# Kernel optimization log

Measured on AMD Instinct MI355X. Metric: run time of the kernel, lower is better.

## Reference

```python
import jax, jax.numpy as jnp
import numpy as np

N_EXPERTS = 256
NUM_POINTS = 512
BATCH = 256
SHARE_DIM = 200
BASE_DIM = 20
LABEL_LEN = 2


def setup_inputs() -> dict:
    key = jax.random.key(0)
    ks = jax.random.split(key, 12)
    s_pre = 1.0 / np.sqrt(NUM_POINTS)
    s_share = 1.0 / np.sqrt(NUM_POINTS)
    s_b1 = 1.0 / np.sqrt(SHARE_DIM)
    s_b2 = 1.0 / np.sqrt(BASE_DIM)
    return {
        "x": jax.random.normal(ks[0], (BATCH, NUM_POINTS), dtype=jnp.float32),
        "magnification": jax.random.uniform(ks[1], (N_EXPERTS, BATCH), dtype=jnp.float32),
        # 256 frozen per-expert Linear(num_points, num_points)
        "W_pre": jax.random.uniform(ks[2], (N_EXPERTS, NUM_POINTS, NUM_POINTS), jnp.float32, -s_pre, s_pre),
        "b_pre": jax.random.uniform(ks[3], (N_EXPERTS, NUM_POINTS), jnp.float32, -s_pre, s_pre),
        # shared: Linear(num_points, 200) + SELU
        "W_share": jax.random.uniform(ks[4], (NUM_POINTS, SHARE_DIM), jnp.float32, -s_share, s_share),
        "b_share": jax.random.uniform(ks[5], (SHARE_DIM,), jnp.float32, -s_share, s_share),
        # base: Linear(200,20)+SELU, Linear(20,2)+Softmax(dim=1)
        "W1": jax.random.uniform(ks[6], (SHARE_DIM, BASE_DIM), jnp.float32, -s_b1, s_b1),
        "b1": jax.random.uniform(ks[7], (BASE_DIM,), jnp.float32, -s_b1, s_b1),
        "W2": jax.random.uniform(ks[8], (BASE_DIM, LABEL_LEN), jnp.float32, -s_b2, s_b2),
        "b2": jax.random.uniform(ks[9], (LABEL_LEN,), jnp.float32, -s_b2, s_b2),
    }


def reference(x, magnification, W_pre, b_pre, W_share, b_share, W1, b1, W2, b2):
    # Batch all 256 expert evaluations as one grouped computation.
    # temp[e,b,p] = magnification[e,b] * x[b,p]
    temp = magnification[:, :, None] * x[None, :, :]            # [E,B,P]
    # per-expert frozen linear: grouped GEMM
    h = jnp.einsum("ebp,epq->ebq", temp, W_pre) + b_pre[:, None, :]   # [E,B,P]
    # shared Linear + SELU
    h = jax.nn.selu(jnp.einsum("ebp,ps->ebs", h, W_share) + b_share)  # [E,B,200]
    # base head (shared weights, applied per expert)
    h = jax.nn.selu(jnp.einsum("ebs,st->ebt", h, W1) + b1)            # [E,B,20]
    logits = jnp.einsum("ebt,tl->ebl", h, W2) + b2                    # [E,B,2]
    probs = jax.nn.softmax(logits, axis=-1)  # Softmax(dim=1) on each [B,2] block
    # torch.cat along dim 0 over the 256 experts
    return probs.reshape(N_EXPERTS * x.shape[0], LABEL_LEN)
```

## Files before the change

kernel.cpp:

```cpp
#include <hip/hip_runtime.h>
#include <hip/hip_bf16.h>


typedef float  f32x4  __attribute__((ext_vector_type(4)));
typedef __bf16 bf16x8 __attribute__((ext_vector_type(8)));
typedef __bf16 bf16x4 __attribute__((ext_vector_type(4)));
typedef int    i32x2  __attribute__((ext_vector_type(2)));
typedef int    i32x4  __attribute__((ext_vector_type(4)));

#define MFMA16(a, b, c) __builtin_amdgcn_mfma_f32_16x16x32_bf16((a), (b), (c), 0, 0, 0)

static constexpr int NB = 256, NP = 512, NS = 200;

static constexpr int ST_PITCH = 72;
static constexpr int ST_BUF   = 64 * ST_PITCH;
static constexpr int OFF_ST   = 0;
static constexpr int OFF_HT   = 9216;
static constexpr int HT_PITCH = 144;
static constexpr int H2_P     = 232;
static constexpr int OFF_H2   = 0;
static constexpr int OFF_PART = 118784;
static constexpr int SMEM_BYTES = 122880;

#define LGKM_BARRIER()                                        \
    do {                                                      \
        asm volatile("s_waitcnt lgkmcnt(0)" ::: "memory");    \
        __builtin_amdgcn_s_barrier();                         \
    } while (0)


__global__ void prep_xf(const float* __restrict__ x, __bf16* __restrict__ xf) {
    int t   = blockIdx.x * 256 + threadIdx.x;
    int l   = t & 63;
    int r16 = (t >> 6) & 15;
    int k32 = t >> 10;
    const float* src = x + (r16 * 16 + (l & 15)) * NP + k32 * 32 + (l >> 4) * 8;
    bf16x8 v;
#pragma unroll
    for (int e = 0; e < 8; e++) v[e] = (__bf16)src[e];
    *(bf16x8*)(xf + (size_t)t * 8) = v;
}

__global__ void prep_ws(const float* __restrict__ Ws, __bf16* __restrict__ wf) {
    int i = blockIdx.x * 256 + threadIdx.x;
    int e8  = i & 7;
    int l   = (i >> 3) & 63;
    int n16 = (i >> 9) % 14;
    int k32 = (i >> 9) / 14;
    int q = k32 * 32 + (l >> 4) * 8 + e8;
    int s = n16 * 16 + (l & 15);
    float v = (s < NS) ? Ws[q * NS + s] : 0.0f;
    wf[i] = (__bf16)v;
}


#define K_STEP(S, XC, XN, WLD, WUSE)                                          \
    {                                                                         \
        const int s1_ = (S) + 1, s2_ = (S) + 2;                               \
        if (s1_ < 128) {                                                      \
            const int k1_ = s1_ & 15;                                         \
            _Pragma("unroll")                                                 \
            for (int i_ = 0; i_ < 4; i_++)                                    \
                XN[i_] = *(const bf16x8*)(xfw + k1_ * 8192 + i_ * 512);       \
        }                                                                     \
        if (s2_ < 128) {                                                      \
            const int nt2_ = s2_ >> 4, k2_ = s2_ & 15;                        \
            _Pragma("unroll")                                                 \
            for (int i_ = 0; i_ < 4; i_++)                                    \
                WLD[i_] = WpreE[(size_t)(k2_ * 32 + p0 + i_) * NP + nt2_ * 64 + q]; \
        }                                                                     \
        {                                                                     \
            const char* stb_ = smem + OFF_ST + ((S) & 1) * ST_BUF;            \
            bf16x8 bf_[2];                                                    \
            _Pragma("unroll")                                                 \
            for (int j_ = 0; j_ < 2; j_++) {                                  \
                const int q_ = wc * 32 + j_ * 16 + l15;                       \
                union { i32x4 u; bf16x8 b; } cv_;                             \
                i32x2 lo_ = *(const i32x2*)(stb_ + q_ * ST_PITCH + lg * 16);  \
                i32x2 hi_ = *(const i32x2*)(stb_ + q_ * ST_PITCH + lg * 16 + 8); \
                cv_.u = (i32x4){lo_.x, lo_.y, hi_.x, hi_.y};                  \
                bf_[j_] = cv_.b;                                              \
            }                                                                 \
            _Pragma("unroll")                                                 \
            for (int i_ = 0; i_ < 4; i_++)                                    \
                _Pragma("unroll")                                             \
                for (int j_ = 0; j_ < 2; j_++)                                \
                    acc1[i_][j_] = MFMA16(XC[i_], bf_[j_], acc1[i_][j_]);     \
        }                                                                     \
        if (s1_ < 128) {                                                      \
            bf16x4 wv_;                                                       \
            _Pragma("unroll")                                                 \
            for (int i_ = 0; i_ < 4; i_++) wv_[i_] = (__bf16)WUSE[i_];        \
            *(bf16x4*)(smem + OFF_ST + (s1_ & 1) * ST_BUF + q * ST_PITCH + p0 * 2) = wv_; \
        }                                                                     \
        LGKM_BARRIER();                                                       \
    }

__global__ __launch_bounds__(512, 2) void fused_experts(
    const float* __restrict__ mag,
    const float* __restrict__ Wpre,
    const float* __restrict__ bpre,
    const float* __restrict__ bshare,
    const float* __restrict__ W1,
    const float* __restrict__ b1,
    const float* __restrict__ W2,
    const float* __restrict__ b2,
    const __bf16* __restrict__ xf,
    const __bf16* __restrict__ wsf,
    float* __restrict__ out)
{
    __shared__ __align__(16) char smem[SMEM_BYTES];

    const int e    = blockIdx.x;
    const int tid  = threadIdx.x;
    const int lane = tid & 63;
    const int wid  = tid >> 6;
    const int wr   = wid >> 1;
    const int wc   = wid & 1;
    const int l15  = lane & 15;
    const int lg   = lane >> 4;

    const int q  = tid & 63;
    const int p0 = (tid >> 6) * 4;

    const float* WpreE = Wpre + (size_t)e * NP * NP;
    const __bf16* xfw  = xf + (wr * 4 * 64 + lane) * 8;

    f32x4 magv[4];
#pragma unroll
    for (int i = 0; i < 4; i++)
        magv[i] = *(const f32x4*)(mag + e * NB + wr * 64 + i * 16 + lg * 4);

    f32x4 acc2[4][7];
#pragma unroll
    for (int i = 0; i < 4; i++)
#pragma unroll
        for (int j = 0; j < 7; j++) acc2[i][j] = (f32x4){0.f, 0.f, 0.f, 0.f};
    f32x4 acc1[4][2];
#pragma unroll
    for (int i = 0; i < 4; i++)
#pragma unroll
        for (int j = 0; j < 2; j++) acc1[i][j] = (f32x4){0.f, 0.f, 0.f, 0.f};

    bf16x8 XA[4], XB[4];
    float  WEV[4], WOD[4], WT[4];

#pragma unroll
    for (int i = 0; i < 4; i++)
        XA[i] = *(const bf16x8*)(xfw + i * 512);
#pragma unroll
    for (int i = 0; i < 4; i++)
        WT[i]  = WpreE[(size_t)(p0 + i) * NP + q];
#pragma unroll
    for (int i = 0; i < 4; i++)
        WOD[i] = WpreE[(size_t)(32 + p0 + i) * NP + q];
    {
        bf16x4 wv;
#pragma unroll
        for (int i = 0; i < 4; i++) wv[i] = (__bf16)WT[i];
        *(bf16x4*)(smem + OFF_ST + q * ST_PITCH + p0 * 2) = wv;
    }
    LGKM_BARRIER();

    __bf16* ht = (__bf16*)(smem + OFF_HT);

    for (int ss = 0; ss < 128; ss += 2) {
        K_STEP(ss,     XA, XB, WEV, WOD);
        K_STEP(ss + 1, XB, XA, WOD, WEV);

        if ((ss & 15) == 14) {
            const int nt = ss >> 4;

            const float bp0 = bpre[e * NP + nt * 64 + wc * 32 + l15];
            const float bp1 = bpre[e * NP + nt * 64 + wc * 32 + 16 + l15];
#pragma unroll
            for (int j = 0; j < 2; j++) {
                const float bp = j ? bp1 : bp0;
#pragma unroll
                for (int i = 0; i < 4; i++) {
#pragma unroll
                    for (int r = 0; r < 4; r++) {
                        const float h = magv[i][r] * acc1[i][j][r] + bp;
                        ht[(wr * 64 + i * 16 + lg * 4 + r) * 72 + wc * 32 + j * 16 + l15] = (__bf16)h;
                    }
                }
            }
            LGKM_BARRIER();

#pragma unroll
            for (int kk = 0; kk < 2; kk++) {
                bf16x8 wfr[7];
#pragma unroll
                for (int j2 = 0; j2 < 7; j2++)
                    wfr[j2] = *(const bf16x8*)(wsf +
                        (size_t)((((nt * 2 + kk) * 14) + wc * 7 + j2) * 64 + lane) * 8);
                bf16x8 a2[4];
#pragma unroll
                for (int i = 0; i < 4; i++)
                    a2[i] = *(const bf16x8*)(ht + (wr * 64 + i * 16 + l15) * 72 + kk * 32 + lg * 8);
#pragma unroll
                for (int i = 0; i < 4; i++)
#pragma unroll
                    for (int j2 = 0; j2 < 7; j2++)
                        acc2[i][j2] = MFMA16(a2[i], wfr[j2], acc2[i][j2]);
            }

#pragma unroll
            for (int i = 0; i < 4; i++)
#pragma unroll
                for (int j = 0; j < 2; j++) acc1[i][j] = (f32x4){0.f, 0.f, 0.f, 0.f};
        }
    }

    __syncthreads();

    __bf16* h2  = (__bf16*)(smem + OFF_H2);
    float* part = (float*)(smem + OFF_PART);
    const float SC = 1.0507009873554805f;
    const float AL = 1.6732632423543772f;

#pragma unroll
    for (int j2 = 0; j2 < 7; j2++) {
        const int s = wc * 112 + j2 * 16 + l15;
        const float bs = (s < NS) ? bshare[s] : 0.0f;
#pragma unroll
        for (int i = 0; i < 4; i++) {
            const int b0 = wr * 64 + i * 16 + lg * 4;
#pragma unroll
            for (int r = 0; r < 4; r++) {
                float z = acc2[i][j2][r] + bs;
                z = (z > 0.f) ? SC * z : SC * AL * (__expf(z) - 1.f);
                h2[(b0 + r) * H2_P + s] = (__bf16)z;
            }
        }
    }
    __syncthreads();

    {
        const int b  = tid & 255;
        const int th = tid >> 8;
        float u[10];
#pragma unroll
        for (int j = 0; j < 10; j++) u[j] = b1[th * 10 + j];
        for (int s8 = 0; s8 < NS; s8 += 8) {
            bf16x8 hv = *(const bf16x8*)(h2 + b * H2_P + s8);
#pragma unroll
            for (int so = 0; so < 8; so++) {
                const float v = (float)hv[so];
                const float* w1row = W1 + (s8 + so) * 20 + th * 10;
#pragma unroll
                for (int j = 0; j < 10; j++) u[j] = fmaf(v, w1row[j], u[j]);
            }
        }
        float pa = 0.f, pb = 0.f;
#pragma unroll
        for (int j = 0; j < 10; j++) {
            float v = u[j];
            v = (v > 0.f) ? SC * v : SC * AL * (__expf(v) - 1.f);
            const int t = th * 10 + j;
            pa = fmaf(v, W2[t * 2 + 0], pa);
            pb = fmaf(v, W2[t * 2 + 1], pb);
        }
        part[tid * 2 + 0] = pa;
        part[tid * 2 + 1] = pb;
    }
    __syncthreads();

    if (tid < 256) {
        const int b = tid;
        const float l0 = part[b * 2 + 0] + part[(b + 256) * 2 + 0] + b2[0];
        const float l1 = part[b * 2 + 1] + part[(b + 256) * 2 + 1] + b2[1];
        const float mx  = fmaxf(l0, l1);
        const float ex0 = __expf(l0 - mx), ex1 = __expf(l1 - mx);
        const float inv = 1.0f / (ex0 + ex1);
        out[((size_t)e * NB + b) * 2 + 0] = ex0 * inv;
        out[((size_t)e * NB + b) * 2 + 1] = ex1 * inv;
    }
}


extern "C" void kernel_launch(void* const* d_in, const int* in_sizes, int n_in,
                              void* d_out, int out_size, void* d_ws, size_t ws_size,
                              hipStream_t stream) {
    const float* x      = (const float*)d_in[0];
    const float* mag    = (const float*)d_in[1];
    const float* Wpre   = (const float*)d_in[2];
    const float* bpre   = (const float*)d_in[3];
    const float* Wshare = (const float*)d_in[4];
    const float* bshare = (const float*)d_in[5];
    const float* W1     = (const float*)d_in[6];
    const float* b1     = (const float*)d_in[7];
    const float* W2     = (const float*)d_in[8];
    const float* b2     = (const float*)d_in[9];
    float* out = (float*)d_out;

    __bf16* xf  = (__bf16*)d_ws;
    __bf16* wsf = (__bf16*)((char*)d_ws + 262144);

    prep_xf<<<64, 256, 0, stream>>>(x, xf);
    prep_ws<<<448, 256, 0, stream>>>(Wshare, wsf);
    fused_experts<<<256, 512, 0, stream>>>(mag, Wpre, bpre, bshare, W1, b1,
                                           W2, b2, xf, wsf, out);
}
```

Before: 483.4 us.

## Split each expert across two workgroups by batch half and deepen K-steps

```diff
diff --git a/kernel.cpp b/kernel.cpp
--- a/kernel.cpp
+++ b/kernel.cpp
@@ -12,15 +12,14 @@
 
 static constexpr int NB = 256, NP = 512, NS = 200;
 
-static constexpr int ST_PITCH = 72;
-static constexpr int ST_BUF   = 64 * ST_PITCH;
-static constexpr int OFF_ST   = 0;
-static constexpr int OFF_HT   = 9216;
-static constexpr int HT_PITCH = 144;
-static constexpr int H2_P     = 232;
-static constexpr int OFF_H2   = 0;
-static constexpr int OFF_PART = 118784;
-static constexpr int SMEM_BYTES = 122880;
+static constexpr int SLICE   = 4608;
+static constexpr int ST_STEP = 2 * SLICE;
+static constexpr int OFF_ST  = 0;
+static constexpr int OFF_HT  = 18432;
+static constexpr int H2_P    = 232;
+static constexpr int OFF_H2  = 0;
+static constexpr int OFF_PART = 59392;
+static constexpr int SMEM_BYTES = 61440;
 
 #define LGKM_BARRIER()                                        \
     do {                                                      \
@@ -54,30 +53,59 @@
 }
 
 
-#define K_STEP(S, XC, XN, WLD, WUSE)                                          \
+#define X_LOAD(SN, XDST)                                                      \
+    if ((SN) < 64) {                                                          \
+        const int kb_ = ((SN) & 7) * 2;                                       \
+        _Pragma("unroll")                                                     \
+        for (int kk_ = 0; kk_ < 2; kk_++)                                     \
+            _Pragma("unroll")                                                 \
+            for (int i_ = 0; i_ < 4; i_++)                                    \
+                XDST[kk_ * 4 + i_] =                                          \
+                    *(const bf16x8*)(xfw + (kb_ + kk_) * 8192 + i_ * 512);    \
+    }
+
+#define W_GATHER(S2, WDST)                                                    \
+    if ((S2) < 64) {                                                          \
+        const int nt2_ = (S2) >> 3;                                           \
+        const int kb2_ = ((S2) & 7) * 2;                                      \
+        _Pragma("unroll")                                                     \
+        for (int sub_ = 0; sub_ < 2; sub_++)                                  \
+            _Pragma("unroll")                                                 \
+            for (int pp_ = 0; pp_ < 2; pp_++)                                 \
+                _Pragma("unroll")                                             \
+                for (int i_ = 0; i_ < 4; i_++)                                \
+                    WDST[sub_ * 8 + pp_ * 4 + i_] =                           \
+                        WpreE[(size_t)((kb2_ + sub_) * 32 + pp_ * 16 + p0 + i_) * NP \
+                              + nt2_ * 64 + q];                               \
+    }
+
+#define W_WRITE(S1, WSRC)                                                     \
+    if ((S1) < 64) {                                                          \
+        char* wb_ = smem + OFF_ST + ((S1) & 1) * ST_STEP;                     \
+        _Pragma("unroll")                                                     \
+        for (int sub_ = 0; sub_ < 2; sub_++)                                  \
+            _Pragma("unroll")                                                 \
+            for (int pp_ = 0; pp_ < 2; pp_++) {                               \
+                bf16x4 wv_;                                                   \
+                _Pragma("unroll")                                             \
+                for (int i_ = 0; i_ < 4; i_++)                                \
+                    wv_[i_] = (__bf16)WSRC[sub_ * 8 + pp_ * 4 + i_];          \
+                *(bf16x4*)(wb_ + sub_ * SLICE + q * 72 + (pp_ * 16 + p0) * 2) = wv_; \
+            }                                                                 \
+    }
+
+#define STEP_MFMA(S, XC)                                                      \
     {                                                                         \
-        const int s1_ = (S) + 1, s2_ = (S) + 2;                               \
-        if (s1_ < 128) {                                                      \
-            const int k1_ = s1_ & 15;                                         \
-            _Pragma("unroll")                                                 \
-            for (int i_ = 0; i_ < 4; i_++)                                    \
-                XN[i_] = *(const bf16x8*)(xfw + k1_ * 8192 + i_ * 512);       \
-        }                                                                     \
-        if (s2_ < 128) {                                                      \
-            const int nt2_ = s2_ >> 4, k2_ = s2_ & 15;                        \
-            _Pragma("unroll")                                                 \
-            for (int i_ = 0; i_ < 4; i_++)                                    \
-                WLD[i_] = WpreE[(size_t)(k2_ * 32 + p0 + i_) * NP + nt2_ * 64 + q]; \
-        }                                                                     \
-        {                                                                     \
-            const char* stb_ = smem + OFF_ST + ((S) & 1) * ST_BUF;            \
+        const char* stb_ = smem + OFF_ST + ((S) & 1) * ST_STEP;               \
+        _Pragma("unroll")                                                     \
+        for (int kk_ = 0; kk_ < 2; kk_++) {                                   \
             bf16x8 bf_[2];                                                    \
             _Pragma("unroll")                                                 \
             for (int j_ = 0; j_ < 2; j_++) {                                  \
                 const int q_ = wc * 32 + j_ * 16 + l15;                       \
                 union { i32x4 u; bf16x8 b; } cv_;                             \
-                i32x2 lo_ = *(const i32x2*)(stb_ + q_ * ST_PITCH + lg * 16);  \
-                i32x2 hi_ = *(const i32x2*)(stb_ + q_ * ST_PITCH + lg * 16 + 8); \
+                i32x2 lo_ = *(const i32x2*)(stb_ + kk_ * SLICE + q_ * 72 + lg * 16);     \
+                i32x2 hi_ = *(const i32x2*)(stb_ + kk_ * SLICE + q_ * 72 + lg * 16 + 8); \
                 cv_.u = (i32x4){lo_.x, lo_.y, hi_.x, hi_.y};                  \
                 bf_[j_] = cv_.b;                                              \
             }                                                                 \
@@ -85,18 +113,19 @@
             for (int i_ = 0; i_ < 4; i_++)                                    \
                 _Pragma("unroll")                                             \
                 for (int j_ = 0; j_ < 2; j_++)                                \
-                    acc1[i_][j_] = MFMA16(XC[i_], bf_[j_], acc1[i_][j_]);     \
+                    acc1[i_][j_] = MFMA16(XC[kk_ * 4 + i_], bf_[j_], acc1[i_][j_]); \
         }                                                                     \
-        if (s1_ < 128) {                                                      \
-            bf16x4 wv_;                                                       \
-            _Pragma("unroll")                                                 \
-            for (int i_ = 0; i_ < 4; i_++) wv_[i_] = (__bf16)WUSE[i_];        \
-            *(bf16x4*)(smem + OFF_ST + (s1_ & 1) * ST_BUF + q * ST_PITCH + p0 * 2) = wv_; \
-        }                                                                     \
-        LGKM_BARRIER();                                                       \
-    }
-
-__global__ __launch_bounds__(512, 2) void fused_experts(
+    }
+
+#define K_STEP(S, XC, XN, WC, WN)  \
+    X_LOAD((S) + 1, XN)            \
+    W_GATHER((S) + 2, WN)          \
+    STEP_MFMA(S, XC)               \
+    W_WRITE((S) + 1, WC)           \
+    LGKM_BARRIER();
+
+
+__global__ __launch_bounds__(256, 2) void fused_experts(
     const float* __restrict__ mag,
     const float* __restrict__ Wpre,
     const float* __restrict__ bpre,
@@ -111,7 +140,9 @@
 {
     __shared__ __align__(16) char smem[SMEM_BYTES];
 
-    const int e    = blockIdx.x;
+    const int bid  = blockIdx.x;
+    const int e    = bid & 255;
+    const int mh   = bid >> 8;
     const int tid  = threadIdx.x;
     const int lane = tid & 63;
     const int wid  = tid >> 6;
@@ -120,16 +151,17 @@
     const int l15  = lane & 15;
     const int lg   = lane >> 4;
 
-    const int q  = tid & 63;
-    const int p0 = (tid >> 6) * 4;
+    const int q  = lane;
+    const int p0 = wid * 4;
 
     const float* WpreE = Wpre + (size_t)e * NP * NP;
-    const __bf16* xfw  = xf + (wr * 4 * 64 + lane) * 8;
+    const __bf16* xfw  = xf + ((mh * 8 + wr * 4) * 64 + lane) * 8;
+    __bf16* ht = (__bf16*)(smem + OFF_HT);
 
     f32x4 magv[4];
 #pragma unroll
     for (int i = 0; i < 4; i++)
-        magv[i] = *(const f32x4*)(mag + e * NB + wr * 64 + i * 16 + lg * 4);
+        magv[i] = *(const f32x4*)(mag + e * NB + mh * 128 + wr * 64 + i * 16 + lg * 4);
 
     f32x4 acc2[4][7];
 #pragma unroll
@@ -142,74 +174,67 @@
 #pragma unroll
         for (int j = 0; j < 2; j++) acc1[i][j] = (f32x4){0.f, 0.f, 0.f, 0.f};
 
-    bf16x8 XA[4], XB[4];
-    float  WEV[4], WOD[4], WT[4];
-
-#pragma unroll
-    for (int i = 0; i < 4; i++)
-        XA[i] = *(const bf16x8*)(xfw + i * 512);
-#pragma unroll
-    for (int i = 0; i < 4; i++)
-        WT[i]  = WpreE[(size_t)(p0 + i) * NP + q];
-#pragma unroll
-    for (int i = 0; i < 4; i++)
-        WOD[i] = WpreE[(size_t)(32 + p0 + i) * NP + q];
-    {
-        bf16x4 wv;
-#pragma unroll
-        for (int i = 0; i < 4; i++) wv[i] = (__bf16)WT[i];
-        *(bf16x4*)(smem + OFF_ST + q * ST_PITCH + p0 * 2) = wv;
-    }
+    bf16x8 XA[8], XB[8];
+    float  WA[16], WB[16];
+    bf16x8 wfr[14];
+
+    X_LOAD(0, XA)
+    W_GATHER(0, WA)
+    W_GATHER(1, WB)
+    W_WRITE(0, WA)
     LGKM_BARRIER();
 
-    __bf16* ht = (__bf16*)(smem + OFF_HT);
-
-    for (int ss = 0; ss < 128; ss += 2) {
-        K_STEP(ss,     XA, XB, WEV, WOD);
-        K_STEP(ss + 1, XB, XA, WOD, WEV);
-
-        if ((ss & 15) == 14) {
-            const int nt = ss >> 4;
-
-            const float bp0 = bpre[e * NP + nt * 64 + wc * 32 + l15];
-            const float bp1 = bpre[e * NP + nt * 64 + wc * 32 + 16 + l15];
-#pragma unroll
-            for (int j = 0; j < 2; j++) {
-                const float bp = j ? bp1 : bp0;
-#pragma unroll
-                for (int i = 0; i < 4; i++) {
-#pragma unroll
-                    for (int r = 0; r < 4; r++) {
-                        const float h = magv[i][r] * acc1[i][j][r] + bp;
-                        ht[(wr * 64 + i * 16 + lg * 4 + r) * 72 + wc * 32 + j * 16 + l15] = (__bf16)h;
-                    }
+    for (int nt = 0; nt < 8; ++nt) {
+        const int S0 = nt * 8;
+
+#pragma unroll
+        for (int kk = 0; kk < 2; kk++)
+#pragma unroll
+            for (int j2 = 0; j2 < 7; j2++)
+                wfr[kk * 7 + j2] = *(const bf16x8*)(wsf +
+                    (size_t)((((nt * 2 + kk) * 14) + wc * 7 + j2) * 64 + lane) * 8);
+        const float bp0 = bpre[e * NP + nt * 64 + wc * 32 + l15];
+        const float bp1 = bpre[e * NP + nt * 64 + wc * 32 + 16 + l15];
+
+        K_STEP(S0 + 0, XA, XB, WB, WA)
+        K_STEP(S0 + 1, XB, XA, WA, WB)
+        K_STEP(S0 + 2, XA, XB, WB, WA)
+        K_STEP(S0 + 3, XB, XA, WA, WB)
+        K_STEP(S0 + 4, XA, XB, WB, WA)
+        K_STEP(S0 + 5, XB, XA, WA, WB)
+        K_STEP(S0 + 6, XA, XB, WB, WA)
+        K_STEP(S0 + 7, XB, XA, WA, WB)
+
+#pragma unroll
+        for (int j = 0; j < 2; j++) {
+            const float bp = j ? bp1 : bp0;
+#pragma unroll
+            for (int i = 0; i < 4; i++)
+#pragma unroll
+                for (int r = 0; r < 4; r++) {
+                    const float h = magv[i][r] * acc1[i][j][r] + bp;
+                    ht[(wr * 64 + i * 16 + lg * 4 + r) * 72 + wc * 32 + j * 16 + l15] = (__bf16)h;
                 }
-            }
-            LGKM_BARRIER();
-
-#pragma unroll
-            for (int kk = 0; kk < 2; kk++) {
-                bf16x8 wfr[7];
+        }
+        LGKM_BARRIER();
+
+#pragma unroll
+        for (int kk = 0; kk < 2; kk++) {
+            bf16x8 a2[4];
+#pragma unroll
+            for (int i = 0; i < 4; i++)
+                a2[i] = *(const bf16x8*)(ht + (wr * 64 + i * 16 + l15) * 72 + kk * 32 + lg * 8);
+#pragma unroll
+            for (int i = 0; i < 4; i++)
 #pragma unroll
                 for (int j2 = 0; j2 < 7; j2++)
-                    wfr[j2] = *(const bf16x8*)(wsf +
-                        (size_t)((((nt * 2 + kk) * 14) + wc * 7 + j2) * 64 + lane) * 8);
-                bf16x8 a2[4];
-#pragma unroll
-                for (int i = 0; i < 4; i++)
-                    a2[i] = *(const bf16x8*)(ht + (wr * 64 + i * 16 + l15) * 72 + kk * 32 + lg * 8);
-#pragma unroll
-                for (int i = 0; i < 4; i++)
-#pragma unroll
-                    for (int j2 = 0; j2 < 7; j2++)
-                        acc2[i][j2] = MFMA16(a2[i], wfr[j2], acc2[i][j2]);
-            }
-
-#pragma unroll
-            for (int i = 0; i < 4; i++)
-#pragma unroll
-                for (int j = 0; j < 2; j++) acc1[i][j] = (f32x4){0.f, 0.f, 0.f, 0.f};
-        }
+                    acc2[i][j2] = MFMA16(a2[i], wfr[kk * 7 + j2], acc2[i][j2]);
+        }
+
+#pragma unroll
+        for (int i = 0; i < 4; i++)
+#pragma unroll
+            for (int j = 0; j < 2; j++) acc1[i][j] = (f32x4){0.f, 0.f, 0.f, 0.f};
     }
 
     __syncthreads();
@@ -237,8 +262,8 @@
     __syncthreads();
 
     {
-        const int b  = tid & 255;
-        const int th = tid >> 8;
+        const int b  = tid & 127;
+        const int th = tid >> 7;
         float u[10];
 #pragma unroll
         for (int j = 0; j < 10; j++) u[j] = b1[th * 10 + j];
@@ -266,15 +291,16 @@
     }
     __syncthreads();
 
-    if (tid < 256) {
+    if (tid < 128) {
         const int b = tid;
-        const float l0 = part[b * 2 + 0] + part[(b + 256) * 2 + 0] + b2[0];
-        const float l1 = part[b * 2 + 1] + part[(b + 256) * 2 + 1] + b2[1];
+        const float l0 = part[b * 2 + 0] + part[(b + 128) * 2 + 0] + b2[0];
+        const float l1 = part[b * 2 + 1] + part[(b + 128) * 2 + 1] + b2[1];
         const float mx  = fmaxf(l0, l1);
         const float ex0 = __expf(l0 - mx), ex1 = __expf(l1 - mx);
         const float inv = 1.0f / (ex0 + ex1);
-        out[((size_t)e * NB + b) * 2 + 0] = ex0 * inv;
-        out[((size_t)e * NB + b) * 2 + 1] = ex1 * inv;
+        const size_t g = (size_t)e * NB + mh * 128 + b;
+        out[g * 2 + 0] = ex0 * inv;
+        out[g * 2 + 1] = ex1 * inv;
     }
 }
 
@@ -299,6 +325,6 @@
 
     prep_xf<<<64, 256, 0, stream>>>(x, xf);
     prep_ws<<<448, 256, 0, stream>>>(Wshare, wsf);
-    fused_experts<<<256, 512, 0, stream>>>(mag, Wpre, bpre, bshare, W1, b1,
+    fused_experts<<<512, 256, 0, stream>>>(mag, Wpre, bpre, bshare, W1, b1,
                                            W2, b2, xf, wsf, out);
 }
```

Measured after the change: 1.351 ms. +179.4%, slower.

## Pre-convert W_pre to bf16 MFMA layout and stream via async global-to-LDS ring

Applied to the files above, without the earlier changes.

```diff
diff --git a/kernel.cpp b/kernel.cpp
--- a/kernel.cpp
+++ b/kernel.cpp
@@ -4,24 +4,19 @@
 
 typedef float  f32x4  __attribute__((ext_vector_type(4)));
 typedef __bf16 bf16x8 __attribute__((ext_vector_type(8)));
-typedef __bf16 bf16x4 __attribute__((ext_vector_type(4)));
-typedef int    i32x2  __attribute__((ext_vector_type(2)));
-typedef int    i32x4  __attribute__((ext_vector_type(4)));
 
 #define MFMA16(a, b, c) __builtin_amdgcn_mfma_f32_16x16x32_bf16((a), (b), (c), 0, 0, 0)
 
 static constexpr int NB = 256, NP = 512, NS = 200;
 
-static constexpr int ST_PITCH = 72;
-static constexpr int ST_BUF   = 64 * ST_PITCH;
-static constexpr int OFF_ST   = 0;
-static constexpr int OFF_HT   = 9216;
-static constexpr int HT_PITCH = 144;
+static constexpr int OFF_RING = 0;
+static constexpr int OFF_HT   = 49152;
 static constexpr int H2_P     = 232;
 static constexpr int OFF_H2   = 0;
 static constexpr int OFF_PART = 118784;
 static constexpr int SMEM_BYTES = 122880;
 
+#define VM_WAIT(N) asm volatile("s_waitcnt vmcnt(" #N ")" ::: "memory")
 #define LGKM_BARRIER()                                        \
     do {                                                      \
         asm volatile("s_waitcnt lgkmcnt(0)" ::: "memory");    \
@@ -53,52 +48,149 @@
     wf[i] = (__bf16)v;
 }
 
-
-#define K_STEP(S, XC, XN, WLD, WUSE)                                          \
-    {                                                                         \
-        const int s1_ = (S) + 1, s2_ = (S) + 2;                               \
-        if (s1_ < 128) {                                                      \
-            const int k1_ = s1_ & 15;                                         \
+__global__ __launch_bounds__(256) void prep_w(const float* __restrict__ Wp,
+                                              __bf16* __restrict__ wpb) {
+    __shared__ float tile[128][65];
+    const int blk = blockIdx.x;
+    const int e   = blk >> 5;
+    const int sb  = blk & 31;
+    const int nt  = sb >> 2;
+    const int kq  = sb & 3;
+    const int t   = threadIdx.x;
+    const int pr  = t >> 4;
+    const int pc  = (t & 15) * 4;
+    const float* src = Wp + (size_t)e * 262144 + (size_t)(kq * 128) * 512 + nt * 64;
+#pragma unroll
+    for (int rr = 0; rr < 8; ++rr) {
+        const int p = rr * 16 + pr;
+        f32x4 v = *(const f32x4*)(src + (size_t)p * 512 + pc);
+        tile[p][pc + 0] = v.x; tile[p][pc + 1] = v.y;
+        tile[p][pc + 2] = v.z; tile[p][pc + 3] = v.w;
+    }
+    __syncthreads();
+#pragma unroll
+    for (int ff = 0; ff < 4; ++ff) {
+        const int f   = ff * 256 + t;
+        const int l   = f & 63;
+        const int n16 = (f >> 6) & 3;
+        const int sl  = f >> 8;
+        const int lp  = sl * 32 + (l >> 4) * 8;
+        const int lq  = n16 * 16 + (l & 15);
+        bf16x8 o;
+#pragma unroll
+        for (int ee = 0; ee < 8; ++ee) o[ee] = (__bf16)tile[lp + ee][lq];
+        const size_t s = (size_t)(nt * 16 + kq * 4 + sl);
+        *(bf16x8*)(wpb + ((size_t)e * 128 + s) * 2048 + (size_t)(n16 * 64 + l) * 8) = o;
+    }
+}
+
+
+#define GLL_ISSUE(SG)                                                         \
+    __builtin_amdgcn_global_load_lds(                                         \
+        (const __attribute__((address_space(1))) unsigned int*)(wp + (size_t)(SG) * 8192), \
+        (__attribute__((address_space(3))) unsigned int*)(void*)(smem + OFF_RING + ((SG) % 6) * 8192 + wid * 1024), \
+        16, 0, 0);
+
+#define X_LOAD(SN, XD)                                                        \
+    {                                                                         \
+        const int kb_ = ((SN) & 7) * 2;                                       \
+        _Pragma("unroll")                                                     \
+        for (int kk_ = 0; kk_ < 2; kk_++)                                     \
             _Pragma("unroll")                                                 \
             for (int i_ = 0; i_ < 4; i_++)                                    \
-                XN[i_] = *(const bf16x8*)(xfw + k1_ * 8192 + i_ * 512);       \
-        }                                                                     \
-        if (s2_ < 128) {                                                      \
-            const int nt2_ = s2_ >> 4, k2_ = s2_ & 15;                        \
-            _Pragma("unroll")                                                 \
-            for (int i_ = 0; i_ < 4; i_++)                                    \
-                WLD[i_] = WpreE[(size_t)(k2_ * 32 + p0 + i_) * NP + nt2_ * 64 + q]; \
-        }                                                                     \
-        {                                                                     \
-            const char* stb_ = smem + OFF_ST + ((S) & 1) * ST_BUF;            \
+                XD[kk_ * 4 + i_] =                                            \
+                    *(const bf16x8*)(xfw + (kb_ + kk_) * 8192 + i_ * 512);    \
+    }
+
+#define STEP_MFMA(S, XC)                                                      \
+    {                                                                         \
+        const char* slab_ = smem + OFF_RING + ((S) % 6) * 8192;               \
+        _Pragma("unroll")                                                     \
+        for (int kk_ = 0; kk_ < 2; kk_++) {                                   \
             bf16x8 bf_[2];                                                    \
             _Pragma("unroll")                                                 \
-            for (int j_ = 0; j_ < 2; j_++) {                                  \
-                const int q_ = wc * 32 + j_ * 16 + l15;                       \
-                union { i32x4 u; bf16x8 b; } cv_;                             \
-                i32x2 lo_ = *(const i32x2*)(stb_ + q_ * ST_PITCH + lg * 16);  \
-                i32x2 hi_ = *(const i32x2*)(stb_ + q_ * ST_PITCH + lg * 16 + 8); \
-                cv_.u = (i32x4){lo_.x, lo_.y, hi_.x, hi_.y};                  \
-                bf_[j_] = cv_.b;                                              \
-            }                                                                 \
+            for (int j_ = 0; j_ < 2; j_++)                                    \
+                bf_[j_] = *(const bf16x8*)(slab_ + kk_ * 4096 +               \
+                               (wc * 2 + j_) * 1024 + lane * 16);             \
             _Pragma("unroll")                                                 \
             for (int i_ = 0; i_ < 4; i_++)                                    \
                 _Pragma("unroll")                                             \
                 for (int j_ = 0; j_ < 2; j_++)                                \
-                    acc1[i_][j_] = MFMA16(XC[i_], bf_[j_], acc1[i_][j_]);     \
+                    acc1[i_][j_] = MFMA16(XC[kk_ * 4 + i_], bf_[j_], acc1[i_][j_]); \
         }                                                                     \
-        if (s1_ < 128) {                                                      \
-            bf16x4 wv_;                                                       \
-            _Pragma("unroll")                                                 \
-            for (int i_ = 0; i_ < 4; i_++) wv_[i_] = (__bf16)WUSE[i_];        \
-            *(bf16x4*)(smem + OFF_ST + (s1_ & 1) * ST_BUF + q * ST_PITCH + p0 * 2) = wv_; \
+    }
+
+#define END_SYNC(S)                                                           \
+    {                                                                         \
+        if ((S) <= 58)      VM_WAIT(12);                                      \
+        else if ((S) == 59) VM_WAIT(11);                                      \
+        else if ((S) == 60) VM_WAIT(10);                                      \
+        else if ((S) == 61) VM_WAIT(9);                                       \
+        else if ((S) == 62) VM_WAIT(8);                                       \
+        LGKM_BARRIER();                                                       \
+    }
+
+#define H_PHASE(NT)                                                           \
+    {                                                                         \
+        const int nt_ = (NT);                                                 \
+        const float bp0_ = bpre[e * NP + nt_ * 64 + wc * 32 + l15];           \
+        const float bp1_ = bpre[e * NP + nt_ * 64 + wc * 32 + 16 + l15];      \
+        _Pragma("unroll")                                                     \
+        for (int i_ = 0; i_ < 4; i_++) {                                      \
+            f32x4 mg_ = *(const f32x4*)(mag + e * NB + wr * 64 + i_ * 16 + lg * 4); \
+            _Pragma("unroll")                                                 \
+            for (int r_ = 0; r_ < 4; r_++) {                                  \
+                const int row_ = wr * 64 + i_ * 16 + lg * 4 + r_;             \
+                ht[row_ * 72 + wc * 32 + l15]      = (__bf16)(mg_[r_] * acc1[i_][0][r_] + bp0_); \
+                ht[row_ * 72 + wc * 32 + 16 + l15] = (__bf16)(mg_[r_] * acc1[i_][1][r_] + bp1_); \
+            }                                                                 \
         }                                                                     \
-        LGKM_BARRIER();                                                       \
-    }
-
-__global__ __launch_bounds__(512, 2) void fused_experts(
+    }
+
+#define GEMM2_PHASE(NT)                                                       \
+    {                                                                         \
+        const int nt_ = (NT);                                                 \
+        _Pragma("unroll")                                                     \
+        for (int kk_ = 0; kk_ < 2; kk_++) {                                   \
+            bf16x8 wfr_[7];                                                   \
+            _Pragma("unroll")                                                 \
+            for (int j2_ = 0; j2_ < 7; j2_++)                                 \
+                wfr_[j2_] = *(const bf16x8*)(wsf +                            \
+                    (size_t)((((nt_ * 2 + kk_) * 14) + wc * 7 + j2_) * 64 + lane) * 8); \
+            bf16x8 a2_[4];                                                    \
+            _Pragma("unroll")                                                 \
+            for (int i_ = 0; i_ < 4; i_++)                                    \
+                a2_[i_] = *(const bf16x8*)(ht + (wr * 64 + i_ * 16 + l15) * 72 + kk_ * 32 + lg * 8); \
+            _Pragma("unroll")                                                 \
+            for (int i_ = 0; i_ < 4; i_++)                                    \
+                _Pragma("unroll")                                             \
+                for (int j2_ = 0; j2_ < 7; j2_++)                             \
+                    acc2[i_][j2_] = MFMA16(a2_[i_], wfr_[j2_], acc2[i_][j2_]); \
+        }                                                                     \
+        _Pragma("unroll")                                                     \
+        for (int i_ = 0; i_ < 4; i_++)                                        \
+            _Pragma("unroll")                                                 \
+            for (int j_ = 0; j_ < 2; j_++)                                    \
+                acc1[i_][j_] = (f32x4){0.f, 0.f, 0.f, 0.f};                   \
+    }
+
+#define K_STEP(S, XC, XN)                                                     \
+    {                                                                         \
+        if ((S) <= 62) { X_LOAD((S) + 1, XN) }                                \
+        if ((S) <= 58) { GLL_ISSUE((S) + 5) }                                 \
+        STEP_MFMA(S, XC)                                                      \
+        if (((S) & 7) == 7) {                                                 \
+            H_PHASE((S) >> 3)                                                 \
+            END_SYNC(S)                                                       \
+            GEMM2_PHASE((S) >> 3)                                             \
+        } else {                                                              \
+            END_SYNC(S)                                                       \
+        }                                                                     \
+    }
+
+
+__global__ __launch_bounds__(512) void fused_experts(
     const float* __restrict__ mag,
-    const float* __restrict__ Wpre,
     const float* __restrict__ bpre,
     const float* __restrict__ bshare,
     const float* __restrict__ W1,
@@ -107,6 +199,7 @@
     const float* __restrict__ b2,
     const __bf16* __restrict__ xf,
     const __bf16* __restrict__ wsf,
+    const __bf16* __restrict__ wpb,
     float* __restrict__ out)
 {
     __shared__ __align__(16) char smem[SMEM_BYTES];
@@ -120,16 +213,10 @@
     const int l15  = lane & 15;
     const int lg   = lane >> 4;
 
-    const int q  = tid & 63;
-    const int p0 = (tid >> 6) * 4;
-
-    const float* WpreE = Wpre + (size_t)e * NP * NP;
-    const __bf16* xfw  = xf + (wr * 4 * 64 + lane) * 8;
-
-    f32x4 magv[4];
-#pragma unroll
-    for (int i = 0; i < 4; i++)
-        magv[i] = *(const f32x4*)(mag + e * NB + wr * 64 + i * 16 + lg * 4);
+    const char* wp = (const char*)wpb + (size_t)e * 524288
+                     + (wid >> 2) * 4096 + (wid & 3) * 1024 + lane * 16;
+    const __bf16* xfw = xf + ((wr * 4) * 64 + lane) * 8;
+    __bf16* ht = (__bf16*)(smem + OFF_HT);
 
     f32x4 acc2[4][7];
 #pragma unroll
@@ -142,74 +229,16 @@
 #pragma unroll
         for (int j = 0; j < 2; j++) acc1[i][j] = (f32x4){0.f, 0.f, 0.f, 0.f};
 
-    bf16x8 XA[4], XB[4];
-    float  WEV[4], WOD[4], WT[4];
-
-#pragma unroll
-    for (int i = 0; i < 4; i++)
-        XA[i] = *(const bf16x8*)(xfw + i * 512);
-#pragma unroll
-    for (int i = 0; i < 4; i++)
-        WT[i]  = WpreE[(size_t)(p0 + i) * NP + q];
-#pragma unroll
-    for (int i = 0; i < 4; i++)
-        WOD[i] = WpreE[(size_t)(32 + p0 + i) * NP + q];
-    {
-        bf16x4 wv;
-#pragma unroll
-        for (int i = 0; i < 4; i++) wv[i] = (__bf16)WT[i];
-        *(bf16x4*)(smem + OFF_ST + q * ST_PITCH + p0 * 2) = wv;
-    }
+    bf16x8 XA[8], XB[8];
+
+    GLL_ISSUE(0) GLL_ISSUE(1) GLL_ISSUE(2) GLL_ISSUE(3) GLL_ISSUE(4)
+    X_LOAD(0, XA)
+    VM_WAIT(12);
     LGKM_BARRIER();
 
-    __bf16* ht = (__bf16*)(smem + OFF_HT);
-
-    for (int ss = 0; ss < 128; ss += 2) {
-        K_STEP(ss,     XA, XB, WEV, WOD);
-        K_STEP(ss + 1, XB, XA, WOD, WEV);
-
-        if ((ss & 15) == 14) {
-            const int nt = ss >> 4;
-
-            const float bp0 = bpre[e * NP + nt * 64 + wc * 32 + l15];
-            const float bp1 = bpre[e * NP + nt * 64 + wc * 32 + 16 + l15];
-#pragma unroll
-            for (int j = 0; j < 2; j++) {
-                const float bp = j ? bp1 : bp0;
-#pragma unroll
-                for (int i = 0; i < 4; i++) {
-#pragma unroll
-                    for (int r = 0; r < 4; r++) {
-                        const float h = magv[i][r] * acc1[i][j][r] + bp;
-                        ht[(wr * 64 + i * 16 + lg * 4 + r) * 72 + wc * 32 + j * 16 + l15] = (__bf16)h;
-                    }
-                }
-            }
-            LGKM_BARRIER();
-
-#pragma unroll
-            for (int kk = 0; kk < 2; kk++) {
-                bf16x8 wfr[7];
-#pragma unroll
-                for (int j2 = 0; j2 < 7; j2++)
-                    wfr[j2] = *(const bf16x8*)(wsf +
-                        (size_t)((((nt * 2 + kk) * 14) + wc * 7 + j2) * 64 + lane) * 8);
-                bf16x8 a2[4];
-#pragma unroll
-                for (int i = 0; i < 4; i++)
-                    a2[i] = *(const bf16x8*)(ht + (wr * 64 + i * 16 + l15) * 72 + kk * 32 + lg * 8);
-#pragma unroll
-                for (int i = 0; i < 4; i++)
-#pragma unroll
-                    for (int j2 = 0; j2 < 7; j2++)
-                        acc2[i][j2] = MFMA16(a2[i], wfr[j2], acc2[i][j2]);
-            }
-
-#pragma unroll
-            for (int i = 0; i < 4; i++)
-#pragma unroll
-                for (int j = 0; j < 2; j++) acc1[i][j] = (f32x4){0.f, 0.f, 0.f, 0.f};
-        }
+    for (int Sp = 0; Sp < 64; Sp += 2) {
+        K_STEP(Sp,     XA, XB)
+        K_STEP(Sp + 1, XB, XA)
     }
 
     __syncthreads();
@@ -296,9 +325,11 @@
 
     __bf16* xf  = (__bf16*)d_ws;
     __bf16* wsf = (__bf16*)((char*)d_ws + 262144);
-
-    prep_xf<<<64, 256, 0, stream>>>(x, xf);
-    prep_ws<<<448, 256, 0, stream>>>(Wshare, wsf);
-    fused_experts<<<256, 512, 0, stream>>>(mag, Wpre, bpre, bshare, W1, b1,
-                                           W2, b2, xf, wsf, out);
-}
+    __bf16* wpb = (__bf16*)((char*)d_ws + 524288);
+
+    prep_w <<<8192, 256, 0, stream>>>(Wpre, wpb);
+    prep_xf<<<64,   256, 0, stream>>>(x, xf);
+    prep_ws<<<448,  256, 0, stream>>>(Wshare, wsf);
+    fused_experts<<<256, 512, 0, stream>>>(mag, bpre, bshare, W1, b1, W2, b2,
+                                           xf, wsf, wpb, out);
+}
```

Measured after the change: 519.2 us. +7.4%, slower.
